# Kernel tuning notes

Hardware: AMD Instinct MI355X
Metric: run time of the kernel (lower is better)

The kernel has to match this reference:

```python
import jax, jax.numpy as jnp
import numpy as np

B, N, D, H = 1, 4096, 1024, 16
K = D // H
ROPE_BASE = 10000.0


def _rope_cos_sin(n, k, base, dtype):
    # GPT-NeoX style rotary embedding: inv_freq over even dims, emb = cat(freqs, freqs)
    inv_freq = 1.0 / (base ** (jnp.arange(0, k, 2, dtype=jnp.float32) / k))  # [K/2]
    pos = jnp.arange(n, dtype=jnp.float32)
    freqs = pos[:, None] * inv_freq[None, :]              # [N, K/2]
    emb = jnp.concatenate([freqs, freqs], axis=-1)        # [N, K]
    return jnp.cos(emb).astype(dtype), jnp.sin(emb).astype(dtype)


def _rotate_half(x):
    x1, x2 = jnp.split(x, 2, axis=-1)
    return jnp.concatenate([-x2, x1], axis=-1)


def setup_inputs() -> dict:
    key = jax.random.key(0)
    kx, kq, ko = jax.random.split(key, 3)
    x = jax.random.normal(kx, (B, N, D), dtype=jnp.float32)
    # torch Linear weights: [out_features, in_features], y = x @ W^T
    w_qkv = jax.random.normal(kq, (3 * H * K, D), dtype=jnp.float32) / np.sqrt(D)
    w_out = jax.random.normal(ko, (D, D), dtype=jnp.float32) / np.sqrt(D)
    return {"x": x, "w_qkv": w_qkv, "w_out": w_out}


def reference(x, w_qkv, w_out):
    b, n, d = x.shape
    qkv = jnp.einsum('bnd,ed->bne', x, w_qkv).reshape(b, n, 3, H, K)
    q, k, v = qkv[:, :, 0], qkv[:, :, 1], qkv[:, :, 2]   # [B, N, H, K]
    cos, sin = _rope_cos_sin(n, K, ROPE_BASE, x.dtype)    # [N, K]
    cos = cos[None, :, None, :]
    sin = sin[None, :, None, :]
    q = q * cos + _rotate_half(q) * sin
    k = k * cos + _rotate_half(k) * sin
    # explicit O(N^2) score matrix, as in the original module
    scores = jnp.einsum('bnhk,bmhk->bnhm', q, k) / np.sqrt(K).astype(x.dtype)
    causal_mask = jnp.tril(jnp.ones((n, n), dtype=bool))  # [N, M]
    scores = jnp.where(causal_mask[None, :, None, :], scores, jnp.finfo(x.dtype).min)
    probs = jax.nn.softmax(scores, axis=-1)
    attn = jnp.einsum('bnhm,bmhk->bnhk', probs, v).reshape(b, n, d)
    return jnp.einsum('bnd,ed->bne', attn, w_out)
```

## Files before the change

### kernel.cpp

```cpp
#include <hip/hip_runtime.h>
#include <hip/hip_bf16.h>
#include <math.h>

#define N_SEQ 4096
#define DIM   1024
#define NHEAD 16
#define HDIM  64
#define E3    3072

typedef short bf16x8 __attribute__((ext_vector_type(8)));
typedef float f32x4  __attribute__((ext_vector_type(4)));
typedef unsigned int u32;

#if __has_builtin(__builtin_amdgcn_exp2f)
#define EXP2(x) __builtin_amdgcn_exp2f(x)
#else
#define EXP2(x) exp2f(x)
#endif

__device__ __forceinline__ float bf2f(unsigned short u) {
    union { unsigned int i; float f; } x; x.i = ((unsigned int)u) << 16; return x.f;
}
__device__ __forceinline__ unsigned short f2bf(float f) {
    union { float f; unsigned int i; } x; x.f = f;
    unsigned int r = x.i + 0x7FFF + ((x.i >> 16) & 1);
    return (unsigned short)(r >> 16);
}
__device__ __forceinline__ unsigned short f2bf_fast(float f) {
    union { float f; unsigned int i; } x; x.f = f;
    return (unsigned short)((x.i + 0x8000u) >> 16);
}
__device__ __forceinline__ f32x4 mfma16(bf16x8 a, bf16x8 b, f32x4 c) {
    return __builtin_amdgcn_mfma_f32_16x16x32_bf16(a, b, c, 0, 0, 0);
}
__device__ __forceinline__ void gload_lds16(const unsigned short* g, unsigned short* l) {
    __builtin_amdgcn_global_load_lds(
        (const __attribute__((address_space(1))) u32*)g,
        (__attribute__((address_space(3))) u32*)l, 16, 0, 0);
}

__device__ __forceinline__ int probe_isf32(const unsigned short* __restrict__ X) {
    __shared__ int cnt;
    if (threadIdx.x == 0) cnt = 0;
    __syncthreads();
    int bad = 0;
    for (int i = threadIdx.x; i < 4096; i += 256) {
        float v = bf2f(X[i]);
        if (!(fabsf(v) < 1e10f)) bad = 1;
    }
    if (bad) atomicAdd(&cnt, 1);
    __syncthreads();
    return cnt > 0;
}

__global__ __launch_bounds__(256)
void prep_kernel(const void* __restrict__ X, const void* __restrict__ Wq,
                 const void* __restrict__ Wo,
                 unsigned short* __restrict__ Xb, unsigned short* __restrict__ Wqb,
                 unsigned short* __restrict__ Wob,
                 int* __restrict__ flag)
{
    const int isf32 = probe_isf32((const unsigned short*)X);
    if (blockIdx.x == 0 && threadIdx.x == 0) *flag = isf32;
    if (!isf32) return;

    const int nX4  = (N_SEQ * DIM) >> 2;
    const int nWq4 = (E3 * DIM) >> 2;
    const int nWo4 = (DIM * DIM) >> 2;
    const int total = nX4 + nWq4 + nWo4;
    const int stride = gridDim.x * blockDim.x;
    for (int i = blockIdx.x * blockDim.x + threadIdx.x; i < total; i += stride) {
        const float4* src; ushort4* dst; int j = i;
        if (j < nX4)                { src = (const float4*)X  + j;  dst = (ushort4*)Xb  + j; }
        else if ((j -= nX4) < nWq4) { src = (const float4*)Wq + j;  dst = (ushort4*)Wqb + j; }
        else { j -= nWq4;             src = (const float4*)Wo + j;  dst = (ushort4*)Wob + j; }
        float4 v = *src;
        ushort4 u;
        u.x = f2bf(v.x); u.y = f2bf(v.y); u.z = f2bf(v.z); u.w = f2bf(v.w);
        *dst = u;
    }
}

__global__ __launch_bounds__(256)
void qkv_mfma_kernel(const void* __restrict__ Xo, const unsigned short* __restrict__ Xc,
                     const void* __restrict__ Wo_, const unsigned short* __restrict__ Wc,
                     const int* __restrict__ flag,
                     unsigned short* __restrict__ Qf,
                     unsigned short* __restrict__ Kf,
                     unsigned short* __restrict__ Vf)
{
    __shared__ __align__(16) unsigned short SMEM[4][4096];

    const int isf32 = *flag;
    const unsigned short* Xb = isf32 ? Xc : (const unsigned short*)Xo;
    const unsigned short* Wb = isf32 ? Wc : (const unsigned short*)Wo_;

    const int tid  = threadIdx.x;
    const int lane = tid & 63;
    const int wave = tid >> 6;
    const int wr = wave >> 1, wc = wave & 1;
    const int lm = lane & 15, q4 = lane >> 4;
    const int rbase = blockIdx.y * 128;
    const int cbase = blockIdx.x * 128;

    const int srow = wave * 16 + (lane >> 2);
    const int scol = (lane & 3) * 8;

    const unsigned short* xsrc = Xb + (size_t)(rbase + srow) * DIM + scol;
    const unsigned short* wsrc = Wb + (size_t)(cbase + srow) * DIM + scol;
    const int la = (wr*64 + lm)*32 + q4*8;
    const int lb = (wc*64 + lm)*32 + q4*8;

    f32x4 acc[4][4];
    #pragma unroll
    for (int i = 0; i < 4; ++i)
        #pragma unroll
        for (int j = 0; j < 4; ++j) acc[i][j] = (f32x4){0.f, 0.f, 0.f, 0.f};

    #define QSTAGE(buf)                                                             \
        {                                                                           \
            _Pragma("unroll")                                                       \
            for (int j = 0; j < 2; ++j) {                                           \
                gload_lds16(xsrc + (size_t)j*64*DIM, &SMEM[buf][j*2048 + wave*512]);   \
                gload_lds16(wsrc + (size_t)j*64*DIM, &SMEM[2+buf][j*2048 + wave*512]); \
            }                                                                       \
            xsrc += 32; wsrc += 32;                                                 \
        }

    QSTAGE(0)
    for (int it = 0; it < DIM/32; ++it) {
        const int cur = it & 1;
        __syncthreads();
        if (it + 1 < DIM/32) QSTAGE(cur ^ 1)

        bf16x8 a[4], b[4];
        #pragma unroll
        for (int mi = 0; mi < 4; ++mi)
            a[mi] = *(const bf16x8*)&SMEM[cur][la + mi*512];
        #pragma unroll
        for (int ni = 0; ni < 4; ++ni)
            b[ni] = *(const bf16x8*)&SMEM[2+cur][lb + ni*512];
        #pragma unroll
        for (int mi = 0; mi < 4; ++mi)
            #pragma unroll
            for (int ni = 0; ni < 4; ++ni)
                acc[mi][ni] = mfma16(a[mi], b[ni], acc[mi][ni]);
    }
    #undef QSTAGE

    __syncthreads();

    const int ecol = cbase + wc * 64;
    const int part = ecol >> 10;
    const int h    = (ecol >> 6) & 15;
    unsigned short* ep = &SMEM[0][0] + wave*4096;

    if (part == 2) {
        #pragma unroll
        for (int mh = 0; mh < 2; ++mh) {
            #pragma unroll
            for (int mi2 = 0; mi2 < 2; ++mi2) {
                const int mi = mh*2 + mi2;
                #pragma unroll
                for (int r = 0; r < 4; ++r) {
                    const int n31 = mi2*16 + q4*4 + r;
                    #pragma unroll
                    for (int ni = 0; ni < 4; ++ni)
                        ep[(ni*16 + lm)*40 + n31] = f2bf(acc[mi][ni][r]);
                }
            }
            const int nb = rbase + wr*64 + mh*32;
            const size_t vb = (((size_t)h*128 + (nb >> 5)) << 11) + (size_t)lane*8;
            #pragma unroll
            for (int ni = 0; ni < 4; ++ni) {
                const bf16x8 fr = *(const bf16x8*)(ep + (ni*16 + lm)*40 + q4*8);
                *(bf16x8*)(Vf + vb + (size_t)ni*512) = fr;
            }
        }
    } else {
        unsigned short* dst = (part == 0) ? Qf : Kf;
        const float scl = (part == 0) ? 0.180336884f : 1.0f;
        const float inv0 = powf(10000.f, -((float)lm)        * (1.f/32.f));
        const float inv1 = powf(10000.f, -((float)(lm + 16)) * (1.f/32.f));
        #pragma unroll
        for (int mi = 0; mi < 4; ++mi) {
            const int tn = rbase + wr*64 + mi*16;
            #pragma unroll
            for (int r = 0; r < 4; ++r) {
                const int n = tn + q4*4 + r;
                float s0, c0, s1, c1;
                sincosf((float)n * inv0, &s0, &c0);
                sincosf((float)n * inv1, &s1, &c1);
                const int row = (q4*4 + r)*72;
                ep[row + lm]      = f2bf((acc[mi][0][r]*c0 - acc[mi][2][r]*s0) * scl);
                ep[row + lm + 16] = f2bf((acc[mi][1][r]*c1 - acc[mi][3][r]*s1) * scl);
                ep[row + lm + 32] = f2bf((acc[mi][2][r]*c0 + acc[mi][0][r]*s0) * scl);
                ep[row + lm + 48] = f2bf((acc[mi][3][r]*c1 + acc[mi][1][r]*s1) * scl);
            }
            const size_t tb = (((size_t)(h*256 + (tn >> 4))) << 10) + (size_t)lane*8;
            #pragma unroll
            for (int c = 0; c < 2; ++c) {
                const bf16x8 fr = *(const bf16x8*)(ep + lm*72 + c*32 + q4*8);
                *(bf16x8*)(dst + tb + (size_t)c*512) = fr;
            }
        }
    }
}

__global__ __launch_bounds__(256, 5)
void attn_mfma_kernel(const unsigned short* __restrict__ Qf,
                      const unsigned short* __restrict__ Kf,
                      const unsigned short* __restrict__ Vf,
                      unsigned short* __restrict__ Attn)
{
    __shared__ __align__(16) unsigned short P16[4][32][40];
    __shared__ __align__(16) float Ox[2][32][64];
    __shared__ float Lx[2][32];

    const int tid  = threadIdx.x;
    const int lane = tid & 63;
    const int wave = tid >> 6;
    const int q4 = lane >> 4, lm = lane & 15;
    const int qh = wave >> 1, kh = wave & 1;

    const int h  = blockIdx.x & 15;
    const int qb = blockIdx.x >> 4;
    const int q0 = (63 - qb) << 6;
    const int qw = q0 + (qh << 5);

    const unsigned short* qp = Qf + (((size_t)(h*256 + (qw >> 4))) << 10) + (size_t)lane * 8;
    bf16x8 aq[2][2];
    aq[0][0] = *(const bf16x8*)(qp);
    aq[0][1] = *(const bf16x8*)(qp + 512);
    aq[1][0] = *(const bf16x8*)(qp + 1024);
    aq[1][1] = *(const bf16x8*)(qp + 1536);

    float l_part[2][4];
    f32x4 o[2][4];
    #pragma unroll
    for (int qi = 0; qi < 2; ++qi) {
        #pragma unroll
        for (int r = 0; r < 4; ++r) l_part[qi][r] = 0.f;
        #pragma unroll
        for (int dc = 0; dc < 4; ++dc) o[qi][dc] = (f32x4){0.f, 0.f, 0.f, 0.f};
    }

    const size_t hb = ((size_t)h) << 18;
    const unsigned short* kc = Kf + hb + (size_t)(kh*2048) + (size_t)lane*8;
    const unsigned short* vc = Vf + hb + (size_t)(kh*2048) + (size_t)lane*8;

    unsigned short* pw  = &P16[wave][0][0];
    unsigned short* pwa = pw + (4*q4)*40 + lm;
    const unsigned short* par = pw + lm*40 + q4*8;

    const int ntiles = (q0 >> 6) + 1;

    for (int it = 0; it < ntiles; ++it) {
        const int kt = it << 6;

        bf16x8 bk[2][2];
        #pragma unroll
        for (int ki = 0; ki < 2; ++ki) {
            bk[ki][0] = *(const bf16x8*)(kc + ki*1024);
            bk[ki][1] = *(const bf16x8*)(kc + ki*1024 + 512);
        }

        f32x4 s[2][2];
        #pragma unroll
        for (int ki = 0; ki < 2; ++ki) {
            #pragma unroll
            for (int qi = 0; qi < 2; ++qi) {
                f32x4 z = (f32x4){0.f, 0.f, 0.f, 0.f};
                z = mfma16(aq[qi][0], bk[ki][0], z);
                s[qi][ki] = mfma16(aq[qi][1], bk[ki][1], z);
            }
        }

        if (kt + 32*kh + 31 > qw) {
            #pragma unroll
            for (int ki = 0; ki < 2; ++ki) {
                const int key = kt + 32*kh + 16*ki + lm;
                #pragma unroll
                for (int qi = 0; qi < 2; ++qi) {
                    const int qq = qw + 16*qi + 4*q4;
                    #pragma unroll
                    for (int r = 0; r < 4; ++r)
                        if (key > qq + r) s[qi][ki][r] = -INFINITY;
                }
            }
        }

        #pragma unroll
        for (int qi = 0; qi < 2; ++qi)
            #pragma unroll
            for (int ki = 0; ki < 2; ++ki)
                #pragma unroll
                for (int r = 0; r < 4; ++r) {
                    const float p = EXP2(s[qi][ki][r]);
                    l_part[qi][r] += p;
                    pwa[qi*640 + r*40 + ki*16] = f2bf_fast(p);
                }

        bf16x8 bv[4];
        #pragma unroll
        for (int dc = 0; dc < 4; ++dc)
            bv[dc] = *(const bf16x8*)(vc + dc*512);

        bf16x8 pa[2];
        pa[0] = *(const bf16x8*)(par);
        pa[1] = *(const bf16x8*)(par + 640);

        #pragma unroll
        for (int dc = 0; dc < 4; ++dc) {
            #pragma unroll
            for (int qi = 0; qi < 2; ++qi)
                o[qi][dc] = mfma16(pa[qi], bv[dc], o[qi][dc]);
        }

        kc += 4096;
        vc += 4096;
    }

    #pragma unroll
    for (int qi = 0; qi < 2; ++qi)
        #pragma unroll
        for (int r = 0; r < 4; ++r) {
            float l = l_part[qi][r];
            #pragma unroll
            for (int mk = 1; mk <= 8; mk <<= 1) l += __shfl_xor(l, mk);
            l_part[qi][r] = l;
        }

    if (kh == 1) {
        #pragma unroll
        for (int qi = 0; qi < 2; ++qi) {
            #pragma unroll
            for (int r = 0; r < 4; ++r) {
                const int qq = 16*qi + 4*q4 + r;
                #pragma unroll
                for (int dc = 0; dc < 4; ++dc)
                    Ox[qh][qq][16*dc + lm] = o[qi][dc][r];
                if (lm == 0) Lx[qh][qq] = l_part[qi][r];
            }
        }
    }
    __syncthreads();
    if (kh == 0) {
        #pragma unroll
        for (int qi = 0; qi < 2; ++qi)
            #pragma unroll
            for (int r = 0; r < 4; ++r) {
                const int qq = 16*qi + 4*q4 + r;
                const float inv = 1.f / (l_part[qi][r] + Lx[qh][qq]);
                const size_t row = (size_t)(qw + qq) * DIM + (h << 6) + lm;
                #pragma unroll
                for (int dc = 0; dc < 4; ++dc) {
                    const float v = o[qi][dc][r] + Ox[qh][qq][16*dc + lm];
                    Attn[row + 16*dc] = f2bf(v * inv);
                }
            }
    }
}

__global__ __launch_bounds__(256)
void out_mfma_kernel(const unsigned short* __restrict__ Ab,
                     const void* __restrict__ Wo_, const unsigned short* __restrict__ Wc,
                     const int* __restrict__ flag,
                     void* __restrict__ Out)
{
    __shared__ unsigned short As[2][4096];
    __shared__ unsigned short Bs[2][2048];

    const int isf32 = *flag;
    const unsigned short* Wb = isf32 ? Wc : (const unsigned short*)Wo_;

    const int tid  = threadIdx.x;
    const int lane = tid & 63;
    const int wave = tid >> 6;
    const int lm = lane & 15, q4 = lane >> 4;
    const int rbase = blockIdx.y * 128;
    const int cbase = blockIdx.x * 64;

    const int srow16 = lane >> 2;
    const int scol = (lane & 3) * 8;

    const unsigned short* asrc = Ab + (size_t)(rbase + wave*32 + srow16) * DIM + scol;
    const unsigned short* bsrc = Wb + (size_t)(cbase + wave*16 + srow16) * DIM + scol;
    const int la = (wave*32 + lm)*32 + q4*8;
    const int lb = lm*32 + q4*8;

    f32x4 acc[2][4];
    #pragma unroll
    for (int i = 0; i < 2; ++i)
        #pragma unroll
        for (int j = 0; j < 4; ++j) acc[i][j] = (f32x4){0.f, 0.f, 0.f, 0.f};

    #define OSTAGE(buf)                                                          \
        {                                                                        \
            _Pragma("unroll")                                                    \
            for (int j = 0; j < 2; ++j)                                          \
                gload_lds16(asrc + (size_t)j*16*DIM, &As[buf][(wave*32 + j*16)*32]); \
            gload_lds16(bsrc, &Bs[buf][(wave*16)*32]);                           \
            asrc += 32; bsrc += 32;                                              \
        }

    OSTAGE(0)
    for (int it = 0; it < DIM/32; ++it) {
        const int cur = it & 1;
        __syncthreads();
        if (it + 1 < DIM/32) OSTAGE(cur ^ 1)

        bf16x8 a[2], b[4];
        #pragma unroll
        for (int mi = 0; mi < 2; ++mi)
            a[mi] = *(const bf16x8*)&As[cur][la + mi*512];
        #pragma unroll
        for (int ni = 0; ni < 4; ++ni)
            b[ni] = *(const bf16x8*)&Bs[cur][lb + ni*512];
        #pragma unroll
        for (int mi = 0; mi < 2; ++mi)
            #pragma unroll
            for (int ni = 0; ni < 4; ++ni)
                acc[mi][ni] = mfma16(a[mi], b[ni], acc[mi][ni]);
    }
    #undef OSTAGE

    #pragma unroll
    for (int mi = 0; mi < 2; ++mi)
        #pragma unroll
        for (int r = 0; r < 4; ++r) {
            const size_t n = rbase + wave*32 + mi*16 + q4*4 + r;
            #pragma unroll
            for (int ni = 0; ni < 4; ++ni) {
                const size_t e = cbase + ni*16 + lm;
                const float v = acc[mi][ni][r];
                if (isf32) ((float*)Out)[n * DIM + e] = v;
                else       ((unsigned short*)Out)[n * DIM + e] = f2bf(v);
            }
        }
}

extern "C" void kernel_launch(void* const* d_in, const int* in_sizes, int n_in,
                              void* d_out, int out_size, void* d_ws, size_t ws_size,
                              hipStream_t stream) {
    const void* X    = d_in[0];
    const void* Wqkv = d_in[1];
    const void* Wout = d_in[2];

    int* flag = (int*)d_ws;
    unsigned short* base = (unsigned short*)((char*)d_ws + 256);
    const size_t nX = (size_t)N_SEQ * DIM;
    const size_t nWq = (size_t)E3 * DIM;
    const size_t nWo = (size_t)DIM * DIM;
    unsigned short* Xb  = base;
    unsigned short* Wqb = Xb + nX;
    unsigned short* Wob = Wqb + nWq;
    unsigned short* Qf  = Wob + nWo;
    unsigned short* Kf  = Qf + nX;
    unsigned short* Vf  = Kf + nX;
    unsigned short* At  = Vf + nX;

    prep_kernel<<<768, 256, 0, stream>>>(X, Wqkv, Wout, Xb, Wqb, Wob, flag);
    qkv_mfma_kernel<<<dim3(E3 / 128, N_SEQ / 128), 256, 0, stream>>>(X, Xb, Wqkv, Wqb, flag, Qf, Kf, Vf);
    attn_mfma_kernel<<<dim3(NHEAD * (N_SEQ / 64)), 256, 0, stream>>>(Qf, Kf, Vf, At);
    out_mfma_kernel<<<dim3(DIM / 64, N_SEQ / 128), 256, 0, stream>>>(At, Wout, Wob, flag, d_out);
}
```

Baseline: 214.4 us.

## Pair mirrored causal query tiles per block to balance work and share K/V loads

Each attention block now handles two query tiles, p and 63-p, for one head, so every block does the same amount of causal work. The two tiles reuse a single stream of K/V fragment loads, and the grid halves to 512 blocks. The next K tile is prefetched into registers one iteration ahead, and the launch-bounds occupancy hint drops from 5 to 2 to make room for the doubled accumulators. The cost is much higher register and LDS use per block, and the prefetch on the last iteration reads just past the end of the head's K slice.

```diff
diff --git a/kernel.cpp b/kernel.cpp
--- a/kernel.cpp
+++ b/kernel.cpp
@@ -207,13 +207,13 @@
     }
 }
 
-__global__ __launch_bounds__(256, 5)
+__global__ __launch_bounds__(256, 2)
 void attn_mfma_kernel(const unsigned short* __restrict__ Qf,
                       const unsigned short* __restrict__ Kf,
                       const unsigned short* __restrict__ Vf,
                       unsigned short* __restrict__ Attn)
 {
-    __shared__ __align__(16) unsigned short P16[4][32][40];
+    __shared__ __align__(16) unsigned short P16[4][2][32][40];
     __shared__ __align__(16) float Ox[2][32][64];
     __shared__ float Lx[2][32];
 
@@ -223,69 +223,99 @@
     const int q4 = lane >> 4, lm = lane & 15;
     const int qh = wave >> 1, kh = wave & 1;
 
-    const int h  = blockIdx.x & 15;
-    const int qb = blockIdx.x >> 4;
-    const int q0 = (63 - qb) << 6;
-    const int qw = q0 + (qh << 5);
-
-    const unsigned short* qp = Qf + (((size_t)(h*256 + (qw >> 4))) << 10) + (size_t)lane * 8;
-    bf16x8 aq[2][2];
-    aq[0][0] = *(const bf16x8*)(qp);
-    aq[0][1] = *(const bf16x8*)(qp + 512);
-    aq[1][0] = *(const bf16x8*)(qp + 1024);
-    aq[1][1] = *(const bf16x8*)(qp + 1536);
-
-    float l_part[2][4];
-    f32x4 o[2][4];
+    const int h = blockIdx.x & 15;
+    const int p = blockIdx.x >> 4;
+    const int qwA = (p << 6) + (qh << 5);
+    const int qwB = ((63 - p) << 6) + (qh << 5);
+    const int ntA = p + 1;
+    const int ntB = 64 - p;
+
+    const unsigned short* qpA = Qf + (((size_t)(h*256 + (qwA >> 4))) << 10) + (size_t)lane * 8;
+    const unsigned short* qpB = Qf + (((size_t)(h*256 + (qwB >> 4))) << 10) + (size_t)lane * 8;
+    bf16x8 aqA[2][2], aqB[2][2];
+    #pragma unroll
+    for (int qi = 0; qi < 2; ++qi)
+        #pragma unroll
+        for (int d = 0; d < 2; ++d) {
+            aqA[qi][d] = *(const bf16x8*)(qpA + qi*1024 + d*512);
+            aqB[qi][d] = *(const bf16x8*)(qpB + qi*1024 + d*512);
+        }
+
+    float lA[2][4], lB[2][4];
+    f32x4 oA[2][4], oB[2][4];
     #pragma unroll
     for (int qi = 0; qi < 2; ++qi) {
         #pragma unroll
-        for (int r = 0; r < 4; ++r) l_part[qi][r] = 0.f;
-        #pragma unroll
-        for (int dc = 0; dc < 4; ++dc) o[qi][dc] = (f32x4){0.f, 0.f, 0.f, 0.f};
+        for (int r = 0; r < 4; ++r) { lA[qi][r] = 0.f; lB[qi][r] = 0.f; }
+        #pragma unroll
+        for (int dc = 0; dc < 4; ++dc) {
+            oA[qi][dc] = (f32x4){0.f, 0.f, 0.f, 0.f};
+            oB[qi][dc] = (f32x4){0.f, 0.f, 0.f, 0.f};
+        }
     }
 
     const size_t hb = ((size_t)h) << 18;
     const unsigned short* kc = Kf + hb + (size_t)(kh*2048) + (size_t)lane*8;
     const unsigned short* vc = Vf + hb + (size_t)(kh*2048) + (size_t)lane*8;
 
-    unsigned short* pw  = &P16[wave][0][0];
-    unsigned short* pwa = pw + (4*q4)*40 + lm;
-    const unsigned short* par = pw + lm*40 + q4*8;
-
-    const int ntiles = (q0 >> 6) + 1;
-
-    for (int it = 0; it < ntiles; ++it) {
+    unsigned short* pwA  = &P16[wave][0][0][0];
+    unsigned short* pwB  = &P16[wave][1][0][0];
+    unsigned short* pwaA = pwA + (4*q4)*40 + lm;
+    unsigned short* pwaB = pwB + (4*q4)*40 + lm;
+    const unsigned short* parA = pwA + lm*40 + q4*8;
+    const unsigned short* parB = pwB + lm*40 + q4*8;
+
+    bf16x8 bk[2][2];
+    bk[0][0] = *(const bf16x8*)(kc);
+    bk[0][1] = *(const bf16x8*)(kc + 512);
+    bk[1][0] = *(const bf16x8*)(kc + 1024);
+    bk[1][1] = *(const bf16x8*)(kc + 1536);
+
+    for (int it = 0; it < ntB; ++it) {
         const int kt = it << 6;
-
-        bf16x8 bk[2][2];
-        #pragma unroll
-        for (int ki = 0; ki < 2; ++ki) {
-            bk[ki][0] = *(const bf16x8*)(kc + ki*1024);
-            bk[ki][1] = *(const bf16x8*)(kc + ki*1024 + 512);
-        }
-
-        f32x4 s[2][2];
-        #pragma unroll
-        for (int ki = 0; ki < 2; ++ki) {
+        const int doA = (it < ntA);
+
+        bf16x8 bv[4];
+        #pragma unroll
+        for (int dc = 0; dc < 4; ++dc)
+            bv[dc] = *(const bf16x8*)(vc + dc*512);
+
+        bf16x8 nk[2][2];
+        nk[0][0] = *(const bf16x8*)(kc + 4096);
+        nk[0][1] = *(const bf16x8*)(kc + 4096 + 512);
+        nk[1][0] = *(const bf16x8*)(kc + 4096 + 1024);
+        nk[1][1] = *(const bf16x8*)(kc + 4096 + 1536);
+
+        f32x4 sB[2][2], sA[2][2];
+        #pragma unroll
+        for (int ki = 0; ki < 2; ++ki)
             #pragma unroll
             for (int qi = 0; qi < 2; ++qi) {
                 f32x4 z = (f32x4){0.f, 0.f, 0.f, 0.f};
-                z = mfma16(aq[qi][0], bk[ki][0], z);
-                s[qi][ki] = mfma16(aq[qi][1], bk[ki][1], z);
-            }
-        }
-
-        if (kt + 32*kh + 31 > qw) {
+                z = mfma16(aqB[qi][0], bk[ki][0], z);
+                sB[qi][ki] = mfma16(aqB[qi][1], bk[ki][1], z);
+            }
+        if (doA) {
+            #pragma unroll
+            for (int ki = 0; ki < 2; ++ki)
+                #pragma unroll
+                for (int qi = 0; qi < 2; ++qi) {
+                    f32x4 z = (f32x4){0.f, 0.f, 0.f, 0.f};
+                    z = mfma16(aqA[qi][0], bk[ki][0], z);
+                    sA[qi][ki] = mfma16(aqA[qi][1], bk[ki][1], z);
+                }
+        }
+
+        if (kt + 32*kh + 31 > qwB) {
             #pragma unroll
             for (int ki = 0; ki < 2; ++ki) {
                 const int key = kt + 32*kh + 16*ki + lm;
                 #pragma unroll
                 for (int qi = 0; qi < 2; ++qi) {
-                    const int qq = qw + 16*qi + 4*q4;
+                    const int qq = qwB + 16*qi + 4*q4;
                     #pragma unroll
                     for (int r = 0; r < 4; ++r)
-                        if (key > qq + r) s[qi][ki][r] = -INFINITY;
+                        if (key > qq + r) sB[qi][ki][r] = -INFINITY;
                 }
             }
         }
@@ -296,53 +326,87 @@
             for (int ki = 0; ki < 2; ++ki)
                 #pragma unroll
                 for (int r = 0; r < 4; ++r) {
-                    const float p = EXP2(s[qi][ki][r]);
-                    l_part[qi][r] += p;
-                    pwa[qi*640 + r*40 + ki*16] = f2bf_fast(p);
-                }
-
-        bf16x8 bv[4];
-        #pragma unroll
-        for (int dc = 0; dc < 4; ++dc)
-            bv[dc] = *(const bf16x8*)(vc + dc*512);
-
-        bf16x8 pa[2];
-        pa[0] = *(const bf16x8*)(par);
-        pa[1] = *(const bf16x8*)(par + 640);
-
-        #pragma unroll
-        for (int dc = 0; dc < 4; ++dc) {
+                    const float pb = EXP2(sB[qi][ki][r]);
+                    lB[qi][r] += pb;
+                    pwaB[qi*640 + r*40 + ki*16] = f2bf_fast(pb);
+                }
+
+        if (doA) {
+            if (kt + 32*kh + 31 > qwA) {
+                #pragma unroll
+                for (int ki = 0; ki < 2; ++ki) {
+                    const int key = kt + 32*kh + 16*ki + lm;
+                    #pragma unroll
+                    for (int qi = 0; qi < 2; ++qi) {
+                        const int qq = qwA + 16*qi + 4*q4;
+                        #pragma unroll
+                        for (int r = 0; r < 4; ++r)
+                            if (key > qq + r) sA[qi][ki][r] = -INFINITY;
+                    }
+                }
+            }
             #pragma unroll
             for (int qi = 0; qi < 2; ++qi)
-                o[qi][dc] = mfma16(pa[qi], bv[dc], o[qi][dc]);
-        }
-
-        kc += 4096;
-        vc += 4096;
+                #pragma unroll
+                for (int ki = 0; ki < 2; ++ki)
+                    #pragma unroll
+                    for (int r = 0; r < 4; ++r) {
+                        const float pa = EXP2(sA[qi][ki][r]);
+                        lA[qi][r] += pa;
+                        pwaA[qi*640 + r*40 + ki*16] = f2bf_fast(pa);
+                    }
+        }
+
+        {
+            bf16x8 paB[2];
+            paB[0] = *(const bf16x8*)(parB);
+            paB[1] = *(const bf16x8*)(parB + 640);
+            #pragma unroll
+            for (int dc = 0; dc < 4; ++dc)
+                #pragma unroll
+                for (int qi = 0; qi < 2; ++qi)
+                    oB[qi][dc] = mfma16(paB[qi], bv[dc], oB[qi][dc]);
+        }
+        if (doA) {
+            bf16x8 paA[2];
+            paA[0] = *(const bf16x8*)(parA);
+            paA[1] = *(const bf16x8*)(parA + 640);
+            #pragma unroll
+            for (int dc = 0; dc < 4; ++dc)
+                #pragma unroll
+                for (int qi = 0; qi < 2; ++qi)
+                    oA[qi][dc] = mfma16(paA[qi], bv[dc], oA[qi][dc]);
+        }
+
+        kc += 4096; vc += 4096;
+        bk[0][0] = nk[0][0]; bk[0][1] = nk[0][1];
+        bk[1][0] = nk[1][0]; bk[1][1] = nk[1][1];
     }
 
     #pragma unroll
     for (int qi = 0; qi < 2; ++qi)
         #pragma unroll
         for (int r = 0; r < 4; ++r) {
-            float l = l_part[qi][r];
-            #pragma unroll
-            for (int mk = 1; mk <= 8; mk <<= 1) l += __shfl_xor(l, mk);
-            l_part[qi][r] = l;
+            float a = lA[qi][r], b = lB[qi][r];
+            #pragma unroll
+            for (int mk = 1; mk <= 8; mk <<= 1) {
+                a += __shfl_xor(a, mk);
+                b += __shfl_xor(b, mk);
+            }
+            lA[qi][r] = a; lB[qi][r] = b;
         }
 
     if (kh == 1) {
         #pragma unroll
-        for (int qi = 0; qi < 2; ++qi) {
+        for (int qi = 0; qi < 2; ++qi)
             #pragma unroll
             for (int r = 0; r < 4; ++r) {
                 const int qq = 16*qi + 4*q4 + r;
                 #pragma unroll
                 for (int dc = 0; dc < 4; ++dc)
-                    Ox[qh][qq][16*dc + lm] = o[qi][dc][r];
-                if (lm == 0) Lx[qh][qq] = l_part[qi][r];
-            }
-        }
+                    Ox[qh][qq][16*dc + lm] = oA[qi][dc][r];
+                if (lm == 0) Lx[qh][qq] = lA[qi][r];
+            }
     }
     __syncthreads();
     if (kh == 0) {
@@ -351,11 +415,40 @@
             #pragma unroll
             for (int r = 0; r < 4; ++r) {
                 const int qq = 16*qi + 4*q4 + r;
-                const float inv = 1.f / (l_part[qi][r] + Lx[qh][qq]);
-                const size_t row = (size_t)(qw + qq) * DIM + (h << 6) + lm;
+                const float inv = 1.f / (lA[qi][r] + Lx[qh][qq]);
+                const size_t row = (size_t)(qwA + qq) * DIM + (h << 6) + lm;
                 #pragma unroll
                 for (int dc = 0; dc < 4; ++dc) {
-                    const float v = o[qi][dc][r] + Ox[qh][qq][16*dc + lm];
+                    const float v = oA[qi][dc][r] + Ox[qh][qq][16*dc + lm];
+                    Attn[row + 16*dc] = f2bf(v * inv);
+                }
+            }
+    }
+    __syncthreads();
+    if (kh == 1) {
+        #pragma unroll
+        for (int qi = 0; qi < 2; ++qi)
+            #pragma unroll
+            for (int r = 0; r < 4; ++r) {
+                const int qq = 16*qi + 4*q4 + r;
+                #pragma unroll
+                for (int dc = 0; dc < 4; ++dc)
+                    Ox[qh][qq][16*dc + lm] = oB[qi][dc][r];
+                if (lm == 0) Lx[qh][qq] = lB[qi][r];
+            }
+    }
+    __syncthreads();
+    if (kh == 0) {
+        #pragma unroll
+        for (int qi = 0; qi < 2; ++qi)
+            #pragma unroll
+            for (int r = 0; r < 4; ++r) {
+                const int qq = 16*qi + 4*q4 + r;
+                const float inv = 1.f / (lB[qi][r] + Lx[qh][qq]);
+                const size_t row = (size_t)(qwB + qq) * DIM + (h << 6) + lm;
+                #pragma unroll
+                for (int dc = 0; dc < 4; ++dc) {
+                    const float v = oB[qi][dc][r] + Ox[qh][qq][16*dc + lm];
                     Attn[row + 16*dc] = f2bf(v * inv);
                 }
             }
@@ -462,6 +555,6 @@
 
     prep_kernel<<<768, 256, 0, stream>>>(X, Wqkv, Wout, Xb, Wqb, Wob, flag);
     qkv_mfma_kernel<<<dim3(E3 / 128, N_SEQ / 128), 256, 0, stream>>>(X, Xb, Wqkv, Wqb, flag, Qf, Kf, Vf);
-    attn_mfma_kernel<<<dim3(NHEAD * (N_SEQ / 64)), 256, 0, stream>>>(Qf, Kf, Vf, At);
+    attn_mfma_kernel<<<dim3(NHEAD * 32), 256, 0, stream>>>(Qf, Kf, Vf, At);
     out_mfma_kernel<<<dim3(DIM / 64, N_SEQ / 128), 256, 0, stream>>>(At, Wout, Wob, flag, d_out);
 }
```

After: 198.9 us. 7.2% less time.
